# Kernel optimization log

Hardware: AMD Instinct MI355X
Metric: run time of the kernel (lower is better)

Reference implementation:

```python
import jax, jax.numpy as jnp
import numpy as np

B, T, D, H, MLP, WIN = 4, 2048, 768, 12, 3072, 256
HD = D // H


def setup_inputs() -> dict:
    key = jax.random.key(0)
    ks = jax.random.split(key, 9)
    s = 0.02
    return {
        "x": jax.random.normal(ks[0], (B, T, D), jnp.float32),
        "in_proj_w": jax.random.normal(ks[1], (3 * D, D), jnp.float32) * s,
        "in_proj_b": jax.random.normal(ks[2], (3 * D,), jnp.float32) * s,
        "out_w": jax.random.normal(ks[3], (D, D), jnp.float32) * s,
        "out_b": jax.random.normal(ks[4], (D,), jnp.float32) * s,
        "w1": jax.random.normal(ks[5], (MLP, D), jnp.float32) * s,
        "b1": jax.random.normal(ks[6], (MLP,), jnp.float32) * s,
        "w2": jax.random.normal(ks[7], (D, MLP), jnp.float32) * s,
        "b2": jax.random.normal(ks[8], (D,), jnp.float32) * s,
        "ln1_g": jnp.ones((D,), jnp.float32),
        "ln1_b": jnp.zeros((D,), jnp.float32),
        "ln2_g": jnp.ones((D,), jnp.float32),
        "ln2_b": jnp.zeros((D,), jnp.float32),
        "window_size": WIN,
    }


def _layernorm(v, g, b, eps=1e-5):
    m = v.mean(-1, keepdims=True)
    var = ((v - m) ** 2).mean(-1, keepdims=True)
    return (v - m) / jnp.sqrt(var + eps) * g + b


def reference(x, in_proj_w, in_proj_b, out_w, out_b, w1, b1, w2, b2,
              ln1_g, ln1_b, ln2_g, ln2_b, window_size):
    Bx, Tx, Dx = x.shape
    # --- local (banded) multi-head self-attention on norm1(x) ---
    xn = _layernorm(x, ln1_g, ln1_b)
    qkv = xn @ in_proj_w.T + in_proj_b            # [B,T,3D]
    q, k, v = jnp.split(qkv, 3, axis=-1)
    to_heads = lambda t: t.reshape(Bx, Tx, H, HD).transpose(0, 2, 1, 3)  # [B,H,T,hd]
    q, k, v = to_heads(q), to_heads(k), to_heads(v)
    scale = jnp.asarray(1.0 / np.sqrt(HD), x.dtype)
    scores = jnp.einsum('bhqd,bhkd->bhqk', q, k) * scale  # [B,H,T,T]
    idx = jnp.arange(Tx)
    banned = jnp.abs(idx[:, None] - idx[None, :]) > window_size  # True = masked
    scores = jnp.where(banned, -jnp.inf, scores)
    attn = jax.nn.softmax(scores, axis=-1)
    o = jnp.einsum('bhqk,bhkd->bhqd', attn, v)
    o = o.transpose(0, 2, 1, 3).reshape(Bx, Tx, Dx)
    o = o @ out_w.T + out_b
    x = x + o
    # --- MLP block on norm2(x) ---
    xn = _layernorm(x, ln2_g, ln2_b)
    h = jax.nn.gelu(xn @ w1.T + b1, approximate=False)
    x = x + (h @ w2.T + b2)
    return x
```

## Files before the change

kernel.cpp:

```cpp
#include <hip/hip_runtime.h>
#include <hip/hip_bf16.h>

typedef __bf16 bf16;
typedef __bf16 v8bf __attribute__((ext_vector_type(8)));
typedef __bf16 v4bf __attribute__((ext_vector_type(4)));
typedef float  v4f  __attribute__((ext_vector_type(4)));

#define DEVI __device__ __forceinline__

constexpr int Bc   = 4;
constexpr int Tc   = 2048;
constexpr int Dc   = 768;
constexpr int Hc   = 12;
constexpr int HDc  = 64;
constexpr int MLPc = 3072;
constexpr int QKVc = 2304;
constexpr int BTc  = Bc * Tc;

DEVI float b2f(bf16 x) { return (float)x; }
DEVI bf16  f2b(float x) { return (bf16)x; }

#define GLDS(gp, lp) __builtin_amdgcn_global_load_lds( \
    (const __attribute__((address_space(1))) void*)(gp), \
    (__attribute__((address_space(3))) void*)(lp), 16, 0, 0)

__global__ __launch_bounds__(256) void cvt2_kernel(
    const float* __restrict__ s0, bf16* __restrict__ d0, int n0,
    const float* __restrict__ s1, bf16* __restrict__ d1)
{
    int i = blockIdx.x * 256 + threadIdx.x;
    const float* s; bf16* d; int j;
    if (i < n0) { s = s0; d = d0; j = i; }
    else        { s = s1; d = d1; j = i - n0; }
    float4 v = ((const float4*)s)[j];
    v4bf o = { f2b(v.x), f2b(v.y), f2b(v.z), f2b(v.w) };
    ((v4bf*)d)[j] = o;
}

__global__ __launch_bounds__(256) void ln_kernel(
    const float* __restrict__ x, const float* __restrict__ g,
    const float* __restrict__ bt, bf16* __restrict__ out)
{
    const int row = blockIdx.x;
    const int t = threadIdx.x;
    const float* xr = x + (size_t)row * Dc;
    float v[3];
    v[0] = xr[t];
    v[1] = xr[t + 256];
    v[2] = xr[t + 512];
    float s = v[0] + v[1] + v[2];
    float s2 = v[0]*v[0] + v[1]*v[1] + v[2]*v[2];
    #pragma unroll
    for (int off = 32; off > 0; off >>= 1) {
        s  += __shfl_down(s, off);
        s2 += __shfl_down(s2, off);
    }
    __shared__ float red[8];
    const int wave = t >> 6, lane = t & 63;
    if (lane == 0) { red[wave] = s; red[4 + wave] = s2; }
    __syncthreads();
    s  = red[0] + red[1] + red[2] + red[3];
    s2 = red[4] + red[5] + red[6] + red[7];
    const float mean = s * (1.0f / Dc);
    const float var  = s2 * (1.0f / Dc) - mean * mean;
    const float rstd = rsqrtf(var + 1e-5f);
    bf16* orow = out + (size_t)row * Dc;
    #pragma unroll
    for (int i = 0; i < 3; i++) {
        int c = t + i * 256;
        orow[c] = f2b((v[i] - mean) * rstd * g[c] + bt[c]);
    }
}

enum { EPI_QKV = 0, EPI_GELU_BF16 = 1, EPI_RESID_F32 = 2, EPI_ACC_F32 = 3 };

template <int EPI, int TN>
__global__ __launch_bounds__(256) void gemm_bt(
    const bf16* __restrict__ A, const bf16* __restrict__ Bw,
    const float* __restrict__ bias,
    bf16* __restrict__ Cb, float* __restrict__ Cf,
    const float* __restrict__ resf,
    int M, int N, int K, int lda, int ldb)
{
    constexpr int MI = (TN == 128) ? 4 : 2;
    __shared__ __align__(16) bf16 sA[128 * 64];
    __shared__ __align__(16) bf16 sB[TN * 64];
    const int t = threadIdx.x, wave = t >> 6, lane = t & 63;
    const int moff = (TN == 128) ? (wave & 1) * 64 : wave * 32;
    const int noff = (TN == 128) ? (wave >> 1) * 64 : 0;
    const int nx = gridDim.x, ny = gridDim.y;
    const int bid = blockIdx.y * nx + blockIdx.x;
    const int xcd = bid & 7, kk = bid >> 3;
    const int m0 = (xcd * (ny >> 3) + kk / nx) * 128;
    const int n0 = (kk % nx) * TN;
    const bf16* Ag = A + (size_t)m0 * lda;
    const bf16* Bg = Bw + (size_t)n0 * ldb;

    v4f acc[MI][4];
    #pragma unroll
    for (int i = 0; i < MI; i++)
        #pragma unroll
        for (int j = 0; j < 4; j++) acc[i][j] = (v4f)(0.0f);

    for (int k0 = 0; k0 < K; k0 += 64) {
        #pragma unroll
        for (int i = 0; i < 4; i++) {
            int c = i * 256 + t;
            int r = c >> 3, j = (c & 7) ^ (r & 7);
            GLDS(Ag + (size_t)r * lda + k0 + j * 8,
                 &sA[(i * 256 + wave * 64) * 8]);
        }
        #pragma unroll
        for (int i = 0; i < TN / 32; i++) {
            int c = i * 256 + t;
            int r = c >> 3, j = (c & 7) ^ (r & 7);
            GLDS(Bg + (size_t)r * ldb + k0 + j * 8,
                 &sB[(i * 256 + wave * 64) * 8]);
        }
        __syncthreads();
        #pragma unroll
        for (int ks = 0; ks < 2; ks++) {
            const int rq = lane >> 4, rl = lane & 15;
            v8bf a[MI], b[4];
            #pragma unroll
            for (int mi = 0; mi < MI; mi++) {
                const int row = moff + mi * 16 + rl;
                a[mi] = *(const v8bf*)&sA[row * 64 + ((ks * 4 + rq) ^ (row & 7)) * 8];
            }
            #pragma unroll
            for (int ni = 0; ni < 4; ni++) {
                const int row = noff + ni * 16 + rl;
                b[ni] = *(const v8bf*)&sB[row * 64 + ((ks * 4 + rq) ^ (row & 7)) * 8];
            }
            #pragma unroll
            for (int mi = 0; mi < MI; mi++)
                #pragma unroll
                for (int ni = 0; ni < 4; ni++)
                    acc[mi][ni] = __builtin_amdgcn_mfma_f32_16x16x32_bf16(
                        a[mi], b[ni], acc[mi][ni], 0, 0, 0);
        }
        __syncthreads();
    }

    const int rq = lane >> 4, cn = lane & 15;
    #pragma unroll
    for (int mi = 0; mi < MI; mi++)
        #pragma unroll
        for (int ni = 0; ni < 4; ni++) {
            const int col = n0 + noff + ni * 16 + cn;
            const float bv = bias ? bias[col] : 0.0f;
            if constexpr (EPI == EPI_QKV) {
                const int row0 = m0 + moff + mi * 16 + rq * 4;
                if (n0 < 2 * Dc) {
                    bf16* dst = Cb + (col < Dc ? 0 : (size_t)BTc * Dc);
                    const int cadj = col < Dc ? col : col - Dc;
                    const float qs = (col < Dc) ? 0.18033688011112042f : 1.0f;
                    #pragma unroll
                    for (int r = 0; r < 4; r++)
                        dst[(size_t)(row0 + r) * Dc + cadj] = f2b((acc[mi][ni][r] + bv) * qs);
                } else {
                    const int vcol = col - 2 * Dc;
                    const int hh = vcol >> 6, hd = vcol & 63;
                    const int bb = row0 >> 11, t0 = row0 & 2047;
                    v4bf pk;
                    #pragma unroll
                    for (int r = 0; r < 4; r++) pk[r] = f2b(acc[mi][ni][r] + bv);
                    *(v4bf*)(Cb + 2 * (size_t)BTc * Dc +
                             (((size_t)bb * Hc + hh) * HDc + hd) * Tc + t0) = pk;
                }
            } else {
                #pragma unroll
                for (int r = 0; r < 4; r++) {
                    const int row = m0 + moff + mi * 16 + rq * 4 + r;
                    const size_t idx = (size_t)row * N + col;
                    float vv = acc[mi][ni][r] + bv;
                    if constexpr (EPI == EPI_GELU_BF16) {
                        Cb[idx] = f2b(0.5f * vv * (1.0f + erff(vv * 0.70710678118f)));
                    } else if constexpr (EPI == EPI_RESID_F32) {
                        Cf[idx] = vv + resf[idx];
                    } else {
                        Cf[idx] = vv + Cf[idx];
                    }
                }
            }
        }
}

__global__ __launch_bounds__(256, 3) void attn_kernel(
    const bf16* __restrict__ Qb, const bf16* __restrict__ Kb,
    const bf16* __restrict__ Vt, bf16* __restrict__ o,
    const int* __restrict__ winp)
{
    const int bh = blockIdx.x, qt = blockIdx.y;
    const int b = bh / Hc, h = bh % Hc;
    const int q0 = qt * 128;
    const int win = *winp;
    const int t = threadIdx.x, wave = t >> 6, lane = t & 63;
    const int rq = lane >> 4, cn = lane & 15;
    const int qw0 = q0 + wave * 32;

    __shared__ __align__(16) bf16 sK[64 * 64];
    __shared__ __align__(16) bf16 sV[64 * 64];
    __shared__ __align__(16) bf16 sP[4][32 * 64];
    bf16* const sPw = &sP[wave][0];
    const int swz = (cn & 7) << 1;

    const bf16* qp  = Qb + ((size_t)b * Tc) * Dc + h * HDc;
    const bf16* kp  = Kb + ((size_t)b * Tc) * Dc + h * HDc;
    const bf16* vtp = Vt + (size_t)bh * HDc * Tc;

    v8bf qf[2][2];
    #pragma unroll
    for (int ks = 0; ks < 2; ks++)
        #pragma unroll
        for (int mi = 0; mi < 2; mi++)
            qf[ks][mi] = *(const v8bf*)(qp + (size_t)(qw0 + mi * 16 + cn) * Dc
                                        + ks * 32 + rq * 8);

    v4f acc_o[2][4];
    #pragma unroll
    for (int mi = 0; mi < 2; mi++)
        #pragma unroll
        for (int nh = 0; nh < 4; nh++) acc_o[mi][nh] = (v4f)(0.0f);
    float l_part[2] = {0.0f, 0.0f};

    const int wlo = max(0, qw0 - win), whi = min(Tc - 1, qw0 + 31 + win);
    const int klo = max(0, q0 - win) & ~63;
    const int khi = min(Tc - 1, q0 + 127 + win);

    for (int kb0 = klo; kb0 <= khi; kb0 += 64) {
        #pragma unroll
        for (int i = 0; i < 2; i++) {
            int c = i * 256 + t;
            int r = c >> 3, j = (c & 7) ^ (r & 7);
            GLDS(kp + (size_t)(kb0 + r) * Dc + j * 8,
                 &sK[(i * 256 + wave * 64) * 8]);
            GLDS(vtp + (size_t)r * Tc + kb0 + j * 8,
                 &sV[(i * 256 + wave * 64) * 8]);
        }
        __syncthreads();

        if (kb0 + 63 >= wlo && kb0 <= whi) {
            v4f sf[4][2];
            #pragma unroll
            for (int kb = 0; kb < 4; kb++)
                #pragma unroll
                for (int mi = 0; mi < 2; mi++) sf[kb][mi] = (v4f)(0.0f);
            #pragma unroll
            for (int ks = 0; ks < 2; ks++) {
                v8bf kf[4];
                #pragma unroll
                for (int kb = 0; kb < 4; kb++) {
                    const int row = kb * 16 + cn;
                    kf[kb] = *(const v8bf*)&sK[row * 64
                                              + ((ks * 4 + rq) ^ (row & 7)) * 8];
                }
                #pragma unroll
                for (int kb = 0; kb < 4; kb++)
                    #pragma unroll
                    for (int mi = 0; mi < 2; mi++)
                        sf[kb][mi] = __builtin_amdgcn_mfma_f32_16x16x32_bf16(
                            kf[kb], qf[ks][mi], sf[kb][mi], 0, 0, 0);
            }

            const bool need_mask = (kb0 + 63 - qw0 > win) || (qw0 + 31 - kb0 > win);
            #pragma unroll
            for (int kb = 0; kb < 4; kb++)
                #pragma unroll
                for (int mi = 0; mi < 2; mi++) {
                    v4bf pk;
                    #pragma unroll
                    for (int r = 0; r < 4; r++) {
                        float tt = sf[kb][mi][r];
                        if (need_mask) {
                            int ki = kb0 + kb * 16 + rq * 4 + r;
                            int qi = qw0 + mi * 16 + cn;
                            int dd = qi - ki; dd = dd < 0 ? -dd : dd;
                            tt = (dd > win) ? -INFINITY : tt;
                        }
                        float p = exp2f(fminf(tt, 30.0f));
                        l_part[mi] += p;
                        pk[r] = f2b(p);
                    }
                    *(v4bf*)&sPw[(mi * 16 + cn) * 64
                                 + (((kb * 4 + rq) ^ swz) << 2)] = pk;
                }

            #pragma unroll
            for (int ks = 0; ks < 2; ks++) {
                v8bf pa[2], vf[4];
                #pragma unroll
                for (int mi = 0; mi < 2; mi++)
                    pa[mi] = *(const v8bf*)&sPw[(mi * 16 + cn) * 64
                                                + (((ks * 8 + rq * 2) ^ swz) << 2)];
                #pragma unroll
                for (int nh = 0; nh < 4; nh++) {
                    const int row = nh * 16 + cn;
                    vf[nh] = *(const v8bf*)&sV[row * 64
                                               + ((ks * 4 + rq) ^ (row & 7)) * 8];
                }
                #pragma unroll
                for (int mi = 0; mi < 2; mi++)
                    #pragma unroll
                    for (int nh = 0; nh < 4; nh++)
                        acc_o[mi][nh] = __builtin_amdgcn_mfma_f32_16x16x32_bf16(
                            pa[mi], vf[ks * 0 + nh], acc_o[mi][nh], 0, 0, 0);
            }
        }
        __syncthreads();
    }

    #pragma unroll
    for (int mi = 0; mi < 2; mi++) {
        l_part[mi] += __shfl_xor(l_part[mi], 16);
        l_part[mi] += __shfl_xor(l_part[mi], 32);
    }

    bf16* ob = o + ((size_t)b * Tc + qw0) * Dc + h * HDc;
    #pragma unroll
    for (int mi = 0; mi < 2; mi++)
        #pragma unroll
        for (int r = 0; r < 4; r++) {
            const float lv = __shfl(l_part[mi], rq * 4 + r);
            const float invl = 1.0f / lv;
            #pragma unroll
            for (int nh = 0; nh < 4; nh++)
                ob[(size_t)(mi * 16 + rq * 4 + r) * Dc + nh * 16 + cn] =
                    f2b(acc_o[mi][nh][r] * invl);
        }
}

extern "C" void kernel_launch(void* const* d_in, const int* in_sizes, int n_in,
                              void* d_out, int out_size, void* d_ws, size_t ws_size,
                              hipStream_t stream)
{
    const float* x     = (const float*)d_in[0];
    const float* inw   = (const float*)d_in[1];
    const float* inb   = (const float*)d_in[2];
    const float* outw  = (const float*)d_in[3];
    const float* outb  = (const float*)d_in[4];
    const float* w1    = (const float*)d_in[5];
    const float* b1    = (const float*)d_in[6];
    const float* w2    = (const float*)d_in[7];
    const float* b2    = (const float*)d_in[8];
    const float* ln1g  = (const float*)d_in[9];
    const float* ln1b  = (const float*)d_in[10];
    const float* ln2g  = (const float*)d_in[11];
    const float* ln2b  = (const float*)d_in[12];
    const int*   winp  = (const int*)d_in[13];
    float* out = (float*)d_out;

    char* ws = (char*)d_ws;
    constexpr size_t A_OFF   = 0;
    constexpr size_t QKV_OFF = (size_t)BTc * Dc * 2;
    constexpr size_t WA_OFF  = QKV_OFF + 3 * (size_t)BTc * Dc * 2;
    constexpr size_t WS_NEED = WA_OFF + (size_t)(QKVc + Dc) * Dc * 2;
    if (ws_size < WS_NEED) return;

    bf16*  xn     = (bf16*)(ws + A_OFF);
    bf16*  qkvb   = (bf16*)(ws + QKV_OFF);
    bf16*  Qb     = qkvb;
    bf16*  Kb     = qkvb + (size_t)BTc * Dc;
    bf16*  Vt     = qkvb + 2 * (size_t)BTc * Dc;
    bf16*  hbuf   = (bf16*)(ws + QKV_OFF);
    bf16*  wmlp   = (bf16*)(ws + QKV_OFF + (size_t)BTc * (2 * Dc) * 2);
    bf16*  w1_b   = wmlp;
    bf16*  w2_b   = wmlp + (size_t)MLPc * Dc;
    bf16*  wqkv_b = (bf16*)(ws + WA_OFF);
    bf16*  wout_b = wqkv_b + (size_t)QKVc * Dc;

    constexpr int HALF = MLPc / 2;
    constexpr int NQKV4 = QKVc * Dc / 4, NOUT4 = Dc * Dc / 4;
    constexpr int NW14  = MLPc * Dc / 4, NW24  = Dc * MLPc / 4;

    cvt2_kernel<<<(NQKV4 + NOUT4) / 256, 256, 0, stream>>>(
        inw, wqkv_b, NQKV4, outw, wout_b);

    ln_kernel<<<BTc, 256, 0, stream>>>(x, ln1g, ln1b, xn);
    gemm_bt<EPI_QKV, 128><<<dim3(QKVc / 128, BTc / 128), 256, 0, stream>>>(
        xn, wqkv_b, inb, qkvb, nullptr, nullptr, BTc, QKVc, Dc, Dc, Dc);
    attn_kernel<<<dim3(Bc * Hc, Tc / 128), 256, 0, stream>>>(Qb, Kb, Vt, xn, winp);
    cvt2_kernel<<<(NW14 + NW24) / 256, 256, 0, stream>>>(
        w1, w1_b, NW14, w2, w2_b);
    gemm_bt<EPI_RESID_F32, 64><<<dim3(Dc / 64, BTc / 128), 256, 0, stream>>>(
        xn, wout_b, outb, nullptr, out, x, BTc, Dc, Dc, Dc, Dc);
    ln_kernel<<<BTc, 256, 0, stream>>>(out, ln2g, ln2b, xn);

    for (int c = 0; c < 2; c++) {
        const bf16* w1c = w1_b + (size_t)c * HALF * Dc;
        const bf16* w2c = w2_b + (size_t)c * HALF;
        gemm_bt<EPI_GELU_BF16, 128><<<dim3(HALF / 128, BTc / 128), 256, 0, stream>>>(
            xn, w1c, b1 + c * HALF, hbuf, nullptr, nullptr, BTc, HALF, Dc, Dc, Dc);
        gemm_bt<EPI_ACC_F32, 64><<<dim3(Dc / 64, BTc / 128), 256, 0, stream>>>(
            hbuf, w2c, (c == 0) ? b2 : nullptr, nullptr, out, nullptr,
            BTc, Dc, HALF, HALF, MLPc);
    }
}
```

Before: 375.4 us.

## Template GEMM K-tile depth and split MLP chunks over rows instead of hidden dim

Adds a BK template parameter to the GEMM so the narrow N=64 GEMMs (out-proj and second MLP GEMM) use a 128-deep K tile, halving K-loop iterations and barriers at the cost of more LDS. The MLP is now chunked along tokens (M halves) rather than the hidden dimension, so the second GEMM runs over the full K=3072 once per row half and writes output directly instead of accumulating into the fp32 output twice. This removes one read-modify-write pass over the output but gives each launch fewer blocks along M.

```diff
diff --git a/kernel.cpp b/kernel.cpp
--- a/kernel.cpp
+++ b/kernel.cpp
@@ -74,7 +74,7 @@
 
 enum { EPI_QKV = 0, EPI_GELU_BF16 = 1, EPI_RESID_F32 = 2, EPI_ACC_F32 = 3 };
 
-template <int EPI, int TN>
+template <int EPI, int TN, int BK>
 __global__ __launch_bounds__(256) void gemm_bt(
     const bf16* __restrict__ A, const bf16* __restrict__ Bw,
     const float* __restrict__ bias,
@@ -83,8 +83,9 @@
     int M, int N, int K, int lda, int ldb)
 {
     constexpr int MI = (TN == 128) ? 4 : 2;
-    __shared__ __align__(16) bf16 sA[128 * 64];
-    __shared__ __align__(16) bf16 sB[TN * 64];
+    constexpr int CH = BK / 8;
+    __shared__ __align__(16) bf16 sA[128 * BK];
+    __shared__ __align__(16) bf16 sB[TN * BK];
     const int t = threadIdx.x, wave = t >> 6, lane = t & 63;
     const int moff = (TN == 128) ? (wave & 1) * 64 : wave * 32;
     const int noff = (TN == 128) ? (wave >> 1) * 64 : 0;
@@ -102,35 +103,40 @@
         #pragma unroll
         for (int j = 0; j < 4; j++) acc[i][j] = (v4f)(0.0f);
 
-    for (int k0 = 0; k0 < K; k0 += 64) {
-        #pragma unroll
-        for (int i = 0; i < 4; i++) {
+    for (int k0 = 0; k0 < K; k0 += BK) {
+        #pragma unroll
+        for (int i = 0; i < (128 * CH) / 256; i++) {
             int c = i * 256 + t;
-            int r = c >> 3, j = (c & 7) ^ (r & 7);
+            int r = c / CH, l0 = c % CH;
+            int j = ((l0 & 7) ^ (r & 7)) | (l0 & ~7);
             GLDS(Ag + (size_t)r * lda + k0 + j * 8,
                  &sA[(i * 256 + wave * 64) * 8]);
         }
         #pragma unroll
-        for (int i = 0; i < TN / 32; i++) {
+        for (int i = 0; i < (TN * CH) / 256; i++) {
             int c = i * 256 + t;
-            int r = c >> 3, j = (c & 7) ^ (r & 7);
+            int r = c / CH, l0 = c % CH;
+            int j = ((l0 & 7) ^ (r & 7)) | (l0 & ~7);
             GLDS(Bg + (size_t)r * ldb + k0 + j * 8,
                  &sB[(i * 256 + wave * 64) * 8]);
         }
         __syncthreads();
         #pragma unroll
-        for (int ks = 0; ks < 2; ks++) {
+        for (int ks = 0; ks < BK / 32; ks++) {
             const int rq = lane >> 4, rl = lane & 15;
+            const int q = ks * 4 + rq;
             v8bf a[MI], b[4];
             #pragma unroll
             for (int mi = 0; mi < MI; mi++) {
                 const int row = moff + mi * 16 + rl;
-                a[mi] = *(const v8bf*)&sA[row * 64 + ((ks * 4 + rq) ^ (row & 7)) * 8];
+                const int l = ((q & 7) ^ (row & 7)) | (q & ~7);
+                a[mi] = *(const v8bf*)&sA[row * BK + l * 8];
             }
             #pragma unroll
             for (int ni = 0; ni < 4; ni++) {
                 const int row = noff + ni * 16 + rl;
-                b[ni] = *(const v8bf*)&sB[row * 64 + ((ks * 4 + rq) ^ (row & 7)) * 8];
+                const int l = ((q & 7) ^ (row & 7)) | (q & ~7);
+                b[ni] = *(const v8bf*)&sB[row * BK + l * 8];
             }
             #pragma unroll
             for (int mi = 0; mi < MI; mi++)
@@ -304,7 +310,7 @@
                     #pragma unroll
                     for (int nh = 0; nh < 4; nh++)
                         acc_o[mi][nh] = __builtin_amdgcn_mfma_f32_16x16x32_bf16(
-                            pa[mi], vf[ks * 0 + nh], acc_o[mi][nh], 0, 0, 0);
+                            pa[mi], vf[nh], acc_o[mi][nh], 0, 0, 0);
             }
         }
         __syncthreads();
@@ -369,7 +375,7 @@
     bf16*  wqkv_b = (bf16*)(ws + WA_OFF);
     bf16*  wout_b = wqkv_b + (size_t)QKVc * Dc;
 
-    constexpr int HALF = MLPc / 2;
+    constexpr int MHALF = BTc / 2;
     constexpr int NQKV4 = QKVc * Dc / 4, NOUT4 = Dc * Dc / 4;
     constexpr int NW14  = MLPc * Dc / 4, NW24  = Dc * MLPc / 4;
 
@@ -377,22 +383,21 @@
         inw, wqkv_b, NQKV4, outw, wout_b);
 
     ln_kernel<<<BTc, 256, 0, stream>>>(x, ln1g, ln1b, xn);
-    gemm_bt<EPI_QKV, 128><<<dim3(QKVc / 128, BTc / 128), 256, 0, stream>>>(
+    gemm_bt<EPI_QKV, 128, 64><<<dim3(QKVc / 128, BTc / 128), 256, 0, stream>>>(
         xn, wqkv_b, inb, qkvb, nullptr, nullptr, BTc, QKVc, Dc, Dc, Dc);
     attn_kernel<<<dim3(Bc * Hc, Tc / 128), 256, 0, stream>>>(Qb, Kb, Vt, xn, winp);
     cvt2_kernel<<<(NW14 + NW24) / 256, 256, 0, stream>>>(
         w1, w1_b, NW14, w2, w2_b);
-    gemm_bt<EPI_RESID_F32, 64><<<dim3(Dc / 64, BTc / 128), 256, 0, stream>>>(
+    gemm_bt<EPI_RESID_F32, 64, 128><<<dim3(Dc / 64, BTc / 128), 256, 0, stream>>>(
         xn, wout_b, outb, nullptr, out, x, BTc, Dc, Dc, Dc, Dc);
     ln_kernel<<<BTc, 256, 0, stream>>>(out, ln2g, ln2b, xn);
 
-    for (int c = 0; c < 2; c++) {
-        const bf16* w1c = w1_b + (size_t)c * HALF * Dc;
-        const bf16* w2c = w2_b + (size_t)c * HALF;
-        gemm_bt<EPI_GELU_BF16, 128><<<dim3(HALF / 128, BTc / 128), 256, 0, stream>>>(
-            xn, w1c, b1 + c * HALF, hbuf, nullptr, nullptr, BTc, HALF, Dc, Dc, Dc);
-        gemm_bt<EPI_ACC_F32, 64><<<dim3(Dc / 64, BTc / 128), 256, 0, stream>>>(
-            hbuf, w2c, (c == 0) ? b2 : nullptr, nullptr, out, nullptr,
-            BTc, Dc, HALF, HALF, MLPc);
+    for (int r = 0; r < 2; r++) {
+        const bf16* xnr = xn + (size_t)r * MHALF * Dc;
+        float*      outr = out + (size_t)r * MHALF * Dc;
+        gemm_bt<EPI_GELU_BF16, 128, 64><<<dim3(MLPc / 128, MHALF / 128), 256, 0, stream>>>(
+            xnr, w1_b, b1, hbuf, nullptr, nullptr, MHALF, MLPc, Dc, Dc, Dc);
+        gemm_bt<EPI_ACC_F32, 64, 128><<<dim3(Dc / 64, MHALF / 128), 256, 0, stream>>>(
+            hbuf, w2_b, b2, nullptr, outr, nullptr, MHALF, Dc, MLPc, MLPc, MLPc);
     }
 }
```

Result: no change. 381.7 us (+1.7%).
